# Kernel tuning notes

Measured on AMD Instinct MI355X. Metric: run time of the kernel, lower is better.

The kernel has to match this reference:

```python
import jax, jax.numpy as jnp
import numpy as np
import math

B, S, D, H, L, DFF, V = 4, 1024, 512, 8, 4, 2048, 32000
DK = D // H
SPARSITY = 0.3
K = max(1, int(S * SPARSITY))  # 307
EPS = 1e-5


def _layernorm(x, g, b):
    mu = jnp.mean(x, axis=-1, keepdims=True)
    var = jnp.mean(jnp.square(x - mu), axis=-1, keepdims=True)
    return (x - mu) * jax.lax.rsqrt(var + EPS) * g + b


def _scatter_topk(scores, k):
    # scores: [B,H,S,S]. keep top-k per row, others -inf (torch.topk + scatter_)
    vals, idx = jax.lax.top_k(scores, k)
    lead = int(np.prod(scores.shape[:-1]))
    sk = scores.shape[-1]
    sparse = jnp.full((lead, sk), -jnp.inf, dtype=scores.dtype)
    rows = jnp.arange(lead)[:, None]
    sparse = sparse.at[rows, idx.reshape(lead, k)].set(vals.reshape(lead, k))
    return sparse.reshape(scores.shape)


def _forward(x, tok_emb, pos_emb, Wq, bq, Wk, bk, Wv, bv, Wo, bo,
             g1, be1, g2, be2, W1, b1, Wm, bm, W2, b2, Wout, bout):
    h = tok_emb[x] + pos_emb[jnp.arange(S)][None, :, :]  # [B,S,D]
    scale = 1.0 / math.sqrt(DK)
    for l in range(L):
        y = _layernorm(h, g1[l], be1[l])
        q = (y @ Wq[l] + bq[l]).reshape(B, S, H, DK).transpose(0, 2, 1, 3)
        kk = (y @ Wk[l] + bk[l]).reshape(B, S, H, DK).transpose(0, 2, 1, 3)
        v = (y @ Wv[l] + bv[l]).reshape(B, S, H, DK).transpose(0, 2, 1, 3)
        scores = jnp.einsum('bhqd,bhkd->bhqk', q, kk) * scale
        sparse = _scatter_topk(scores, K)
        attn = jax.nn.softmax(sparse, axis=-1)
        o = jnp.einsum('bhqk,bhkd->bhqd', attn, v)
        o = o.transpose(0, 2, 1, 3).reshape(B, S, D) @ Wo[l] + bo[l]
        h = h + o
        z = _layernorm(h, g2[l], be2[l])
        f = jax.nn.gelu(z @ W1[l] + b1[l], approximate=False)
        f = jax.nn.gelu(f @ Wm[l] + bm[l], approximate=False)
        f = f @ W2[l] + b2[l]
        h = h + f
    return h @ Wout + bout  # logits [B,S,V]


def setup_inputs() -> dict:
    key = jax.random.key(0)
    ks = iter(jax.random.split(key, 32))
    xa = lambda shape, fan: (jax.random.normal(next(ks), shape, jnp.float32)
                             * math.sqrt(2.0 / fan))
    return {
        'x': jax.random.randint(next(ks), (B, S), 0, V, dtype=jnp.int32),
        'tok_emb': xa((V, D), V + D),
        'pos_emb': xa((S, D), S + D),
        'Wq': xa((L, D, D), 2 * D), 'bq': jnp.zeros((L, D), jnp.float32),
        'Wk': xa((L, D, D), 2 * D), 'bk': jnp.zeros((L, D), jnp.float32),
        'Wv': xa((L, D, D), 2 * D), 'bv': jnp.zeros((L, D), jnp.float32),
        'Wo': xa((L, D, D), 2 * D), 'bo': jnp.zeros((L, D), jnp.float32),
        'g1': jnp.ones((L, D), jnp.float32), 'be1': jnp.zeros((L, D), jnp.float32),
        'g2': jnp.ones((L, D), jnp.float32), 'be2': jnp.zeros((L, D), jnp.float32),
        'W1': xa((L, D, DFF), D + DFF), 'b1': jnp.zeros((L, DFF), jnp.float32),
        'Wm': xa((L, DFF, DFF), 2 * DFF), 'bm': jnp.zeros((L, DFF), jnp.float32),
        'W2': xa((L, DFF, D), D + DFF), 'b2': jnp.zeros((L, D), jnp.float32),
        'Wout': xa((D, V), D + V), 'bout': jnp.zeros((V,), jnp.float32),
    }


def reference(x, tok_emb, pos_emb, Wq, bq, Wk, bk, Wv, bv, Wo, bo,
              g1, be1, g2, be2, W1, b1, Wm, bm, W2, b2, Wout, bout):
    return _forward(x, tok_emb, pos_emb, Wq, bq, Wk, bk, Wv, bv, Wo, bo,
                    g1, be1, g2, be2, W1, b1, Wm, bm, W2, b2, Wout, bout)
```

## Files before the change

### kernel.cpp

```cpp
#include <hip/hip_runtime.h>
#include <hip/hip_bf16.h>
#include <math.h>

#define B_ 4
#define S_ 1024
#define D_ 512
#define H_ 8
#define L_ 4
#define DFF_ 2048
#define V_ 32000
#define DK_ 64
#define KTOP 307
#define SRS 1048

using bf16x8 = __attribute__((ext_vector_type(8))) __bf16;
using bf16x4 = __attribute__((ext_vector_type(4))) __bf16;
using bf16x2 = __attribute__((ext_vector_type(2))) __bf16;
using f32x4v = __attribute__((ext_vector_type(4))) float;

__device__ __forceinline__ void gload_lds16(const __bf16* g, __bf16* l) {
  __builtin_amdgcn_global_load_lds(
      (const __attribute__((address_space(1))) void*)g,
      (__attribute__((address_space(3))) void*)l, 16, 0, 0);
}

__device__ __forceinline__ unsigned int f32_to_bf16_bits(float s) {
  unsigned int x = __float_as_uint(s);
  return (x + 0x7FFFu + ((x >> 16) & 1u)) >> 16;
}

__device__ __forceinline__ int red16i(int x) {
  x += __builtin_amdgcn_update_dpp(0, x, 0xB1, 0xF, 0xF, true);
  x += __builtin_amdgcn_update_dpp(0, x, 0x4E, 0xF, 0xF, true);
  x += __builtin_amdgcn_update_dpp(0, x, 0x141, 0xF, 0xF, true);
  x += __builtin_amdgcn_update_dpp(0, x, 0x140, 0xF, 0xF, true);
  return x;
}
__device__ __forceinline__ unsigned int red16umax(unsigned int x) {
  unsigned int t;
  t = (unsigned int)__builtin_amdgcn_update_dpp(0, (int)x, 0xB1, 0xF, 0xF, true);  x = t > x ? t : x;
  t = (unsigned int)__builtin_amdgcn_update_dpp(0, (int)x, 0x4E, 0xF, 0xF, true);  x = t > x ? t : x;
  t = (unsigned int)__builtin_amdgcn_update_dpp(0, (int)x, 0x141, 0xF, 0xF, true); x = t > x ? t : x;
  t = (unsigned int)__builtin_amdgcn_update_dpp(0, (int)x, 0x140, 0xF, 0xF, true); x = t > x ? t : x;
  return x;
}
__device__ __forceinline__ float red16f(float x) {
  x += __int_as_float(__builtin_amdgcn_update_dpp(0, __float_as_int(x), 0xB1, 0xF, 0xF, true));
  x += __int_as_float(__builtin_amdgcn_update_dpp(0, __float_as_int(x), 0x4E, 0xF, 0xF, true));
  x += __int_as_float(__builtin_amdgcn_update_dpp(0, __float_as_int(x), 0x141, 0xF, 0xF, true));
  x += __int_as_float(__builtin_amdgcn_update_dpp(0, __float_as_int(x), 0x140, 0xF, 0xF, true));
  return x;
}
__device__ __forceinline__ float red64f(float x) {
  x = red16f(x);
  x += __shfl_xor(x, 16, 64);
  x += __shfl_xor(x, 32, 64);
  return x;
}

template<int ROWS>
__device__ __forceinline__ void stage_tile4(const __bf16* src, int Kd, __bf16* lds,
                                            int w, int lane) {
  #pragma unroll
  for (int c = 0; c < ROWS / 32; ++c) {
    int rblk = (c * 4 + w) * 8;
    int row = rblk + (lane >> 3);
    int col = (lane & 7) * 8;
    int scol = col ^ ((row & 7) << 3);
    gload_lds16(src + (size_t)row * Kd + scol, lds + rblk * 64);
  }
}
__device__ __forceinline__ void stage_half8(const __bf16* src, int Kd, __bf16* lds,
                                            int w, int lane) {
  #pragma unroll
  for (int c = 0; c < 2; ++c) {
    int rblk = (c * 8 + w) * 8;
    int row = rblk + (lane >> 3);
    int col = (lane & 7) * 8;
    int scol = col ^ ((row & 7) << 3);
    gload_lds16(src + (size_t)row * Kd + scol, lds + rblk * 64);
  }
}
__device__ __forceinline__ bf16x8 lds_frag64(const __bf16* lds, int row, int colbase) {
  int col = colbase ^ ((row & 7) << 3);
  return *reinterpret_cast<const bf16x8*>(lds + row * 64 + col);
}

__global__ void embed_kernel(const int* __restrict__ x, const float* __restrict__ tok,
                             const float* __restrict__ pos, float* __restrict__ h) {
  int row = blockIdx.x;
  int t = threadIdx.x;
  int s = row & (S_ - 1);
  int token = x[row];
  const float4* t4 = reinterpret_cast<const float4*>(tok + (size_t)token * D_);
  const float4* p4 = reinterpret_cast<const float4*>(pos + (size_t)s * D_);
  float4 a = t4[t];
  float4 b = p4[t];
  a.x += b.x; a.y += b.y; a.z += b.z; a.w += b.w;
  reinterpret_cast<float4*>(h + (size_t)row * D_)[t] = a;
}

__global__ void ln_kernel(const float* __restrict__ xin, const float* __restrict__ g,
                          const float* __restrict__ bta, __bf16* __restrict__ y) {
  int row = blockIdx.x;
  int t = threadIdx.x;
  const float2* x2 = reinterpret_cast<const float2*>(xin + (size_t)row * D_);
  float2 v = x2[t];
  float s = v.x + v.y;
  float q = v.x * v.x + v.y * v.y;
  s = red64f(s);
  q = red64f(q);
  __shared__ float red[4];
  __shared__ float red2[4];
  int wid = t >> 6, lane = t & 63;
  if (lane == 0) { red[wid] = s; red2[wid] = q; }
  __syncthreads();
  float mu = (red[0] + red[1] + red[2] + red[3]) * (1.0f / D_);
  float ex2 = (red2[0] + red2[1] + red2[2] + red2[3]) * (1.0f / D_);
  float var = ex2 - mu * mu;
  float rstd = rsqrtf(var + 1e-5f);
  float2 gg = reinterpret_cast<const float2*>(g)[t];
  float2 bb = reinterpret_cast<const float2*>(bta)[t];
  bf16x2 o2;
  o2[0] = (__bf16)((v.x - mu) * rstd * gg.x + bb.x);
  o2[1] = (__bf16)((v.y - mu) * rstd * gg.y + bb.y);
  *reinterpret_cast<bf16x2*>(y + (size_t)row * D_ + t * 2) = o2;
}

__global__ void transpose_bf16_kernel(const float* __restrict__ in, __bf16* __restrict__ out,
                                      int Kd, int N, long in_bstride, long out_bstride) {
  __shared__ float tile[32][33];
  const float* ib = in + (size_t)blockIdx.z * in_bstride;
  __bf16* ob = out + (size_t)blockIdx.z * out_bstride;
  int n0 = blockIdx.x * 32, k0 = blockIdx.y * 32;
  int tx = threadIdx.x & 31, ty = threadIdx.x >> 5;
  #pragma unroll
  for (int i = 0; i < 4; ++i)
    tile[ty + i * 8][tx] = ib[(size_t)(k0 + ty + i * 8) * N + n0 + tx];
  __syncthreads();
  #pragma unroll
  for (int i = 0; i < 4; ++i)
    ob[(size_t)(n0 + ty + i * 8) * Kd + k0 + tx] = (__bf16)tile[tx][ty + i * 8];
}

__global__ void concat_bias_kernel(const float* __restrict__ bq, const float* __restrict__ bk,
                                   const float* __restrict__ bv, float* __restrict__ bqkv) {
  int i = blockIdx.x * 256 + threadIdx.x;
  int l = i / 1536, c = i - l * 1536;
  float v = (c < 512) ? bq[l * 512 + c]
          : (c < 1024) ? bk[l * 512 + c - 512]
                       : bv[l * 512 + c - 1024];
  bqkv[i] = v;
}

#define BM 128
#define BN 128
#define BK 64

template<int OMODE, bool GELU_ACT, bool RES, bool SWZ>
__global__ __launch_bounds__(256)
void gemm_bf16_kernel(const __bf16* __restrict__ A, const __bf16* __restrict__ WT,
                      const float* __restrict__ bias, const float* __restrict__ res,
                      void* __restrict__ outp, void* __restrict__ outp2, void* __restrict__ outp3,
                      int M, int N, int Kd) {
  __shared__ __bf16 As[BM * BK];
  __shared__ __bf16 Ws[BN * BK];
  int tid = threadIdx.x;
  int lane = tid & 63, w = tid >> 6;
  int wr = w >> 1, wc = w & 1;
  int lr = lane & 15, lg = lane >> 4;
  int bx, by;
  if (SWZ) {
    int lid = blockIdx.x;
    int cpx = gridDim.x >> 3;
    int swz = (lid & 7) * cpx + (lid >> 3);
    int gx = M >> 7;
    bx = swz % gx;
    by = swz / gx;
  } else {
    bx = blockIdx.x; by = blockIdx.y;
  }
  int row0 = bx * BM, col0 = by * BN;

  const __bf16* Abase = A + (size_t)row0 * Kd;
  const __bf16* Wbase = WT + (size_t)col0 * Kd;

  f32x4v acc[4][4];
  #pragma unroll
  for (int i = 0; i < 4; ++i)
    #pragma unroll
    for (int j = 0; j < 4; ++j)
      #pragma unroll
      for (int e = 0; e < 4; ++e) acc[i][j][e] = 0.0f;

  for (int k0 = 0; k0 < Kd; k0 += BK) {
    stage_tile4<128>(Abase + k0, Kd, As, w, lane);
    stage_tile4<128>(Wbase + k0, Kd, Ws, w, lane);
    __syncthreads();
    bf16x8 af[4][2], bfr[4][2];
    #pragma unroll
    for (int mr = 0; mr < 4; ++mr)
      #pragma unroll
      for (int kk = 0; kk < 2; ++kk)
        af[mr][kk] = lds_frag64(As, wr * 64 + mr * 16 + lr, kk * 32 + lg * 8);
    #pragma unroll
    for (int nc = 0; nc < 4; ++nc)
      #pragma unroll
      for (int kk = 0; kk < 2; ++kk)
        bfr[nc][kk] = lds_frag64(Ws, wc * 64 + nc * 16 + lr, kk * 32 + lg * 8);
    __builtin_amdgcn_s_setprio(1);
    #pragma unroll
    for (int mr = 0; mr < 4; ++mr)
      #pragma unroll
      for (int nc = 0; nc < 4; ++nc) {
        acc[mr][nc] = __builtin_amdgcn_mfma_f32_16x16x32_bf16(af[mr][0], bfr[nc][0], acc[mr][nc], 0, 0, 0);
        acc[mr][nc] = __builtin_amdgcn_mfma_f32_16x16x32_bf16(af[mr][1], bfr[nc][1], acc[mr][nc], 0, 0, 0);
      }
    __builtin_amdgcn_s_setprio(0);
    __syncthreads();
  }

  #pragma unroll
  for (int mr = 0; mr < 4; ++mr) {
    #pragma unroll
    for (int nc = 0; nc < 4; ++nc) {
      int c = col0 + wc * 64 + nc * 16 + lr;
      int rb = row0 + wr * 64 + mr * 16 + lg * 4;
      float vv[4];
      #pragma unroll
      for (int j = 0; j < 4; ++j) {
        float t = acc[mr][nc][j] + bias[c];
        if (RES) t += res[(size_t)(rb + j) * N + c];
        if (GELU_ACT) t = 0.5f * t * (1.0f + erff(t * 0.70710678118654752f));
        vv[j] = t;
      }
      if (OMODE == 0) {
        float* out = (float*)outp;
        #pragma unroll
        for (int j = 0; j < 4; ++j) out[(size_t)(rb + j) * N + c] = vv[j];
      } else if (OMODE == 1) {
        __bf16* out = (__bf16*)outp;
        #pragma unroll
        for (int j = 0; j < 4; ++j) out[(size_t)(rb + j) * N + c] = (__bf16)vv[j];
      } else if (OMODE == 3) {
        float* out = (float*)outp;
        __bf16* out2 = (__bf16*)outp2;
        #pragma unroll
        for (int j = 0; j < 4; ++j) {
          out[(size_t)(rb + j) * N + c] = vv[j];
          out2[(size_t)(rb + j) * N + c] = (__bf16)vv[j];
        }
      }
    }
  }
}

template<int OMODE, bool RES>
__global__ __launch_bounds__(256)
void gemm64_kernel(const __bf16* __restrict__ A, const __bf16* __restrict__ WT,
                   const float* __restrict__ bias, const float* __restrict__ res,
                   void* __restrict__ outp, void* __restrict__ outp2, void* __restrict__ outp3,
                   int M, int N, int Kd) {
  __shared__ __bf16 As[64 * BK];
  __shared__ __bf16 Ws[BN * BK];
  int tid = threadIdx.x;
  int lane = tid & 63, w = tid >> 6;
  int wr = w >> 1, wc = w & 1;
  int lr = lane & 15, lg = lane >> 4;
  int row0 = blockIdx.x * 64, col0 = blockIdx.y * BN;

  const __bf16* Abase = A + (size_t)row0 * Kd;
  const __bf16* Wbase = WT + (size_t)col0 * Kd;

  f32x4v acc[2][4];
  #pragma unroll
  for (int i = 0; i < 2; ++i)
    #pragma unroll
    for (int j = 0; j < 4; ++j)
      #pragma unroll
      for (int e = 0; e < 4; ++e) acc[i][j][e] = 0.0f;

  for (int k0 = 0; k0 < Kd; k0 += BK) {
    stage_tile4<64>(Abase + k0, Kd, As, w, lane);
    stage_tile4<128>(Wbase + k0, Kd, Ws, w, lane);
    __syncthreads();
    bf16x8 af[2][2], bfr[4][2];
    #pragma unroll
    for (int mr = 0; mr < 2; ++mr)
      #pragma unroll
      for (int kk = 0; kk < 2; ++kk)
        af[mr][kk] = lds_frag64(As, wr * 32 + mr * 16 + lr, kk * 32 + lg * 8);
    #pragma unroll
    for (int nc = 0; nc < 4; ++nc)
      #pragma unroll
      for (int kk = 0; kk < 2; ++kk)
        bfr[nc][kk] = lds_frag64(Ws, wc * 64 + nc * 16 + lr, kk * 32 + lg * 8);
    __builtin_amdgcn_s_setprio(1);
    #pragma unroll
    for (int mr = 0; mr < 2; ++mr)
      #pragma unroll
      for (int nc = 0; nc < 4; ++nc) {
        acc[mr][nc] = __builtin_amdgcn_mfma_f32_16x16x32_bf16(af[mr][0], bfr[nc][0], acc[mr][nc], 0, 0, 0);
        acc[mr][nc] = __builtin_amdgcn_mfma_f32_16x16x32_bf16(af[mr][1], bfr[nc][1], acc[mr][nc], 0, 0, 0);
      }
    __builtin_amdgcn_s_setprio(0);
    __syncthreads();
  }

  #pragma unroll
  for (int mr = 0; mr < 2; ++mr) {
    #pragma unroll
    for (int nc = 0; nc < 4; ++nc) {
      int c = col0 + wc * 64 + nc * 16 + lr;
      int rb = row0 + wr * 32 + mr * 16 + lg * 4;
      float vv[4];
      #pragma unroll
      for (int j = 0; j < 4; ++j) {
        float t = acc[mr][nc][j] + bias[c];
        if (RES) t += res[(size_t)(rb + j) * N + c];
        vv[j] = t;
      }
      if (OMODE == 0) {
        float* out = (float*)outp;
        #pragma unroll
        for (int j = 0; j < 4; ++j) out[(size_t)(rb + j) * N + c] = vv[j];
      } else if (OMODE == 3) {
        float* out = (float*)outp;
        __bf16* out2 = (__bf16*)outp2;
        #pragma unroll
        for (int j = 0; j < 4; ++j) {
          out[(size_t)(rb + j) * N + c] = vv[j];
          out2[(size_t)(rb + j) * N + c] = (__bf16)vv[j];
        }
      } else {
        if (col0 < 512) {
          __bf16* out = (__bf16*)outp;
          #pragma unroll
          for (int j = 0; j < 4; ++j) out[(size_t)(rb + j) * D_ + c] = (__bf16)vv[j];
        } else if (col0 < 1024) {
          __bf16* out = (__bf16*)outp2;
          #pragma unroll
          for (int j = 0; j < 4; ++j) out[(size_t)(rb + j) * D_ + (c - 512)] = (__bf16)vv[j];
        } else {
          __bf16* out = (__bf16*)outp3;
          int b = rb >> 10, s0 = rb & (S_ - 1);
          bf16x4 pk;
          #pragma unroll
          for (int j = 0; j < 4; ++j) pk[j] = (__bf16)vv[j];
          *reinterpret_cast<bf16x4*>(&out[((size_t)b * D_ + (c - 1024)) * S_ + s0]) = pk;
        }
      }
    }
  }
}

__global__ __launch_bounds__(512)
void gemm_head_kernel(const __bf16* __restrict__ A, const __bf16* __restrict__ WT,
                      const float* __restrict__ bias, float* __restrict__ out,
                      int M, int N, int Kd) {
  __shared__ __bf16 lds[2][2][256 * 64];
  const int tid = threadIdx.x;
  const int lane = tid & 63, w = tid >> 6;
  const int wr = w >> 2, wc = w & 3;
  const int lr = lane & 15, lg = lane >> 4;

  int lid = blockIdx.x;
  int cpx = gridDim.x >> 3;
  int swz = (lid & 7) * cpx + (lid >> 3);
  int gx = M >> 8;
  int bx = swz % gx, by = swz / gx;
  int row0 = bx * 256, col0 = by * 256;

  const __bf16* Asrc = A + (size_t)row0 * Kd;
  const __bf16* Bsrc = WT + (size_t)col0 * Kd;

  f32x4v acc[8][4];
  #pragma unroll
  for (int i = 0; i < 8; ++i)
    #pragma unroll
    for (int j = 0; j < 4; ++j)
      #pragma unroll
      for (int e = 0; e < 4; ++e) acc[i][j][e] = 0.0f;

  const int NT = Kd / 64;
  stage_half8(Asrc,                      Kd, &lds[0][0][0],    w, lane);
  stage_half8(Asrc + (size_t)128 * Kd,   Kd, &lds[0][0][8192], w, lane);
  stage_half8(Bsrc,                      Kd, &lds[0][1][0],    w, lane);
  stage_half8(Bsrc + (size_t)128 * Kd,   Kd, &lds[0][1][8192], w, lane);

  for (int t = 0; t < NT; ++t) {
    int cur = t & 1, nxt = cur ^ 1;
    int k1 = (t + 1) * 64;
    const __bf16* Ab = &lds[cur][0][0];
    const __bf16* Bb = &lds[cur][1][0];
    bf16x8 bfr[4][2];
    #pragma unroll
    for (int p = 0; p < 4; ++p) {
      if (t < NT - 1) {
        const __bf16* s;
        __bf16* d;
        if (p == 0)      { s = Asrc + k1;                    d = &lds[nxt][0][0]; }
        else if (p == 1) { s = Asrc + (size_t)128 * Kd + k1; d = &lds[nxt][0][8192]; }
        else if (p == 2) { s = Bsrc + k1;                    d = &lds[nxt][1][0]; }
        else             { s = Bsrc + (size_t)128 * Kd + k1; d = &lds[nxt][1][8192]; }
        stage_half8(s, Kd, d, w, lane);
      }
      if (p == 0) {
        if (t < NT - 1) asm volatile("s_waitcnt vmcnt(2)" ::: "memory");
        else            asm volatile("s_waitcnt vmcnt(0)" ::: "memory");
        __builtin_amdgcn_s_barrier();
        #pragma unroll
        for (int nn = 0; nn < 4; ++nn)
          #pragma unroll
          for (int kk = 0; kk < 2; ++kk)
            bfr[nn][kk] = lds_frag64(Bb, wc * 64 + nn * 16 + lr, kk * 32 + lg * 8);
      }
      bf16x8 af[2][2];
      #pragma unroll
      for (int mm = 0; mm < 2; ++mm)
        #pragma unroll
        for (int kk = 0; kk < 2; ++kk)
          af[mm][kk] = lds_frag64(Ab, wr * 128 + p * 32 + mm * 16 + lr, kk * 32 + lg * 8);
      asm volatile("s_waitcnt lgkmcnt(0)" ::: "memory");
      __builtin_amdgcn_sched_barrier(0);
      __builtin_amdgcn_s_setprio(1);
      #pragma unroll
      for (int mm = 0; mm < 2; ++mm)
        #pragma unroll
        for (int nn = 0; nn < 4; ++nn) {
          acc[p * 2 + mm][nn] = __builtin_amdgcn_mfma_f32_16x16x32_bf16(af[mm][0], bfr[nn][0], acc[p * 2 + mm][nn], 0, 0, 0);
          acc[p * 2 + mm][nn] = __builtin_amdgcn_mfma_f32_16x16x32_bf16(af[mm][1], bfr[nn][1], acc[p * 2 + mm][nn], 0, 0, 0);
        }
      __builtin_amdgcn_s_setprio(0);
    }
    __builtin_amdgcn_s_barrier();
  }

  #pragma unroll
  for (int mg = 0; mg < 8; ++mg) {
    #pragma unroll
    for (int nn = 0; nn < 4; ++nn) {
      int c = col0 + wc * 64 + nn * 16 + lr;
      int rb = row0 + wr * 128 + mg * 16 + lg * 4;
      float b = bias[c];
      #pragma unroll
      for (int j = 0; j < 4; ++j)
        out[(size_t)(rb + j) * N + c] = acc[mg][nn][j] + b;
    }
  }
}

__global__ __launch_bounds__(256)
void attn_kernel(const __bf16* __restrict__ qm, const __bf16* __restrict__ km,
                 const __bf16* __restrict__ vt, __bf16* __restrict__ o) {
  __shared__ unsigned short sc16[16][SRS];
  __shared__ float rs[16];
  const int q0 = blockIdx.x * 16;
  const int hh = blockIdx.y;
  const int bb = blockIdx.z;
  const int tid = threadIdx.x;
  const int lane = tid & 63, w = tid >> 6;
  const int lr = lane & 15, lg = lane >> 4;

  const __bf16* qrow = qm + ((size_t)(bb * S_ + q0 + lr)) * D_ + hh * DK_;
  bf16x8 qf0 = *reinterpret_cast<const bf16x8*>(qrow + lg * 8);
  bf16x8 qf1 = *reinterpret_cast<const bf16x8*>(qrow + 32 + lg * 8);

  const __bf16* kbase = km + ((size_t)bb * S_) * D_ + hh * DK_;
  #pragma unroll 8
  for (int kt = 0; kt < 16; ++kt) {
    int key0 = kt * 64 + w * 16;
    const __bf16* krow = kbase + (size_t)(key0 + lr) * D_;
    bf16x8 kf0 = *reinterpret_cast<const bf16x8*>(krow + lg * 8);
    bf16x8 kf1 = *reinterpret_cast<const bf16x8*>(krow + 32 + lg * 8);
    f32x4v d = {0.0f, 0.0f, 0.0f, 0.0f};
    __builtin_amdgcn_s_setprio(1);
    d = __builtin_amdgcn_mfma_f32_16x16x32_bf16(qf0, kf0, d, 0, 0, 0);
    d = __builtin_amdgcn_mfma_f32_16x16x32_bf16(qf1, kf1, d, 0, 0, 0);
    __builtin_amdgcn_s_setprio(0);
    #pragma unroll
    for (int j = 0; j < 4; ++j) {
      unsigned int u = f32_to_bf16_bits(d[j] * 0.125f);
      u = (u & 0x8000u) ? (~u & 0xFFFFu) : (u | 0x8000u);
      sc16[lg * 4 + j][key0 + lr] = (unsigned short)u;
    }
  }
  __syncthreads();

  {
    int r = tid >> 4, tc = tid & 15;
    const unsigned int* srow = reinterpret_cast<const unsigned int*>(&sc16[r][0]);
    unsigned int wv[32];
    #pragma unroll
    for (int g = 0; g < 8; ++g) {
      uint4 t4 = *reinterpret_cast<const uint4*>(&srow[g * 64 + tc * 4]);
      wv[g * 4 + 0] = t4.x; wv[g * 4 + 1] = t4.y;
      wv[g * 4 + 2] = t4.z; wv[g * 4 + 3] = t4.w;
    }
    unsigned int umax = 0;
    #pragma unroll
    for (int i = 0; i < 32; ++i) {
      unsigned int a = wv[i] & 0xFFFFu, b = wv[i] >> 16;
      unsigned int mx = a > b ? a : b;
      umax = mx > umax ? mx : umax;
    }
    umax = red16umax(umax);
    unsigned int lo = 0;
    for (int bit = 15; bit >= 0; --bit) {
      unsigned int cs = (lo | (1u << bit)) << 16;
      int cnt = 0;
      #pragma unroll
      for (int i = 0; i < 32; ++i) {
        cnt += ((wv[i] << 16) >= cs) ? 1 : 0;
        cnt += (wv[i] >= cs) ? 1 : 0;
      }
      cnt = red16i(cnt);
      if (cnt >= KTOP) lo |= (1u << bit);
    }
    unsigned int um = (umax & 0x8000u) ? (umax ^ 0x8000u) : (~umax & 0xFFFFu);
    float mval = __uint_as_float(um << 16);

    __bf16* P = reinterpret_cast<__bf16*>(&sc16[r][0]);
    float lsum = 0.0f;
    #pragma unroll
    for (int g = 0; g < 8; ++g) {
      bf16x8 pk;
      #pragma unroll
      for (int e = 0; e < 8; ++e) {
        unsigned int wrd = wv[g * 4 + (e >> 1)];
        unsigned int u = (e & 1) ? (wrd >> 16) : (wrd & 0xFFFFu);
        float p = 0.0f;
        if (u >= lo) {
          unsigned int ub = (u & 0x8000u) ? (u ^ 0x8000u) : (~u & 0xFFFFu);
          p = __expf(__uint_as_float(ub << 16) - mval);
        }
        pk[e] = (__bf16)p;
        lsum += (float)pk[e];
      }
      *reinterpret_cast<bf16x8*>(&P[tc * 8 + g * 128]) = pk;
    }
    lsum = red16f(lsum);
    if (tc == 0) rs[r] = 1.0f / lsum;
  }
  __syncthreads();

  {
    const __bf16* P0 = reinterpret_cast<const __bf16*>(&sc16[0][0]);
    const __bf16* vbase = vt + ((size_t)bb * D_ + hh * DK_ + w * 16 + lr) * S_;
    const __bf16* prow = P0 + (size_t)lr * SRS;
    f32x4v oacc = {0.0f, 0.0f, 0.0f, 0.0f};
    __builtin_amdgcn_s_setprio(1);
    #pragma unroll 8
    for (int kt = 0; kt < 32; ++kt) {
      bf16x8 a = *reinterpret_cast<const bf16x8*>(prow + kt * 32 + lg * 8);
      bf16x8 b = *reinterpret_cast<const bf16x8*>(vbase + kt * 32 + lg * 8);
      oacc = __builtin_amdgcn_mfma_f32_16x16x32_bf16(a, b, oacc, 0, 0, 0);
    }
    __builtin_amdgcn_s_setprio(0);
    #pragma unroll
    for (int j = 0; j < 4; ++j) {
      int qr = lg * 4 + j;
      float ov = oacc[j] * rs[qr];
      o[((size_t)(bb * S_ + q0 + qr)) * D_ + hh * DK_ + w * 16 + lr] = (__bf16)ov;
    }
  }
}

extern "C" void kernel_launch(void* const* d_in, const int* in_sizes, int n_in,
                              void* d_out, int out_size, void* d_ws, size_t ws_size,
                              hipStream_t stream) {
  (void)in_sizes; (void)n_in; (void)out_size; (void)ws_size;
  const int*   x    = (const int*)d_in[0];
  const float* tok  = (const float*)d_in[1];
  const float* pos  = (const float*)d_in[2];
  const float* Wq   = (const float*)d_in[3];
  const float* bq   = (const float*)d_in[4];
  const float* Wk   = (const float*)d_in[5];
  const float* bk   = (const float*)d_in[6];
  const float* Wv   = (const float*)d_in[7];
  const float* bv   = (const float*)d_in[8];
  const float* Wo   = (const float*)d_in[9];
  const float* bo   = (const float*)d_in[10];
  const float* g1   = (const float*)d_in[11];
  const float* be1  = (const float*)d_in[12];
  const float* g2   = (const float*)d_in[13];
  const float* be2  = (const float*)d_in[14];
  const float* W1   = (const float*)d_in[15];
  const float* b1   = (const float*)d_in[16];
  const float* Wm   = (const float*)d_in[17];
  const float* bm   = (const float*)d_in[18];
  const float* W2   = (const float*)d_in[19];
  const float* b2   = (const float*)d_in[20];
  const float* Wout = (const float*)d_in[21];
  const float* bout = (const float*)d_in[22];
  float* logits = (float*)d_out;

  const int M = B_ * S_;
  float* ws = (float*)d_ws;
  float* h    = ws;
  float* bqkv = h + (size_t)M * D_;
  __bf16* y16  = (__bf16*)(bqkv + (size_t)L_ * 1536);
  __bf16* f1b  = y16  + (size_t)M * D_;
  __bf16* f2b  = f1b  + (size_t)M * DFF_;
  __bf16* qb16 = f2b  + (size_t)M * DFF_;
  __bf16* kb16 = qb16 + (size_t)M * D_;
  __bf16* vt16 = kb16 + (size_t)M * D_;
  __bf16* ob16 = vt16 + (size_t)M * D_;
  __bf16* h16  = ob16 + (size_t)M * D_;
  __bf16* WqkvT = h16 + (size_t)M * D_;
  __bf16* WoT  = WqkvT + (size_t)L_ * 1536 * D_;
  __bf16* W1T  = WoT  + (size_t)L_ * D_ * D_;
  __bf16* WmT  = W1T  + (size_t)L_ * D_ * DFF_;
  __bf16* W2T  = WmT  + (size_t)L_ * DFF_ * DFF_;
  __bf16* WoutT = W2T + (size_t)L_ * D_ * DFF_;

  const long DD = (long)D_ * D_;
  transpose_bf16_kernel<<<dim3(D_/32,  D_/32,   L_), 256, 0, stream>>>(Wq, WqkvT,            D_, D_, DD, 1536L*D_);
  transpose_bf16_kernel<<<dim3(D_/32,  D_/32,   L_), 256, 0, stream>>>(Wk, WqkvT + 512*512,  D_, D_, DD, 1536L*D_);
  transpose_bf16_kernel<<<dim3(D_/32,  D_/32,   L_), 256, 0, stream>>>(Wv, WqkvT + 1024*512, D_, D_, DD, 1536L*D_);
  transpose_bf16_kernel<<<dim3(D_/32,  D_/32,   L_), 256, 0, stream>>>(Wo, WoT, D_, D_, DD, DD);
  transpose_bf16_kernel<<<dim3(DFF_/32, D_/32,  L_), 256, 0, stream>>>(W1, W1T, D_, DFF_, (long)D_*DFF_, (long)D_*DFF_);
  transpose_bf16_kernel<<<dim3(DFF_/32, DFF_/32,L_), 256, 0, stream>>>(Wm, WmT, DFF_, DFF_, (long)DFF_*DFF_, (long)DFF_*DFF_);
  transpose_bf16_kernel<<<dim3(D_/32,  DFF_/32, L_), 256, 0, stream>>>(W2, W2T, DFF_, D_, (long)D_*DFF_, (long)D_*DFF_);
  transpose_bf16_kernel<<<dim3(V_/32,  D_/32,   1 ), 256, 0, stream>>>(Wout, WoutT, D_, V_, (long)D_*V_, (long)D_*V_);
  concat_bias_kernel<<<(L_*1536)/256, 256, 0, stream>>>(bq, bk, bv, bqkv);

  embed_kernel<<<M, 128, 0, stream>>>(x, tok, pos, h);

  for (int l = 0; l < L_; ++l) {
    ln_kernel<<<M, 256, 0, stream>>>(h, g1 + l * D_, be1 + l * D_, y16);
    gemm64_kernel<4,false><<<dim3(M/64, 1536/BN), 256, 0, stream>>>(
        y16, WqkvT + (size_t)l * 1536 * D_, bqkv + l * 1536, nullptr,
        qb16, kb16, vt16, M, 1536, D_);
    attn_kernel<<<dim3(S_/16, H_, B_), 256, 0, stream>>>(qb16, kb16, vt16, ob16);
    gemm64_kernel<0,true><<<dim3(M/64, D_/BN), 256, 0, stream>>>(
        ob16, WoT + (size_t)l * DD, bo + l * D_, h, h, nullptr, nullptr, M, D_, D_);
    ln_kernel<<<M, 256, 0, stream>>>(h, g2 + l * D_, be2 + l * D_, y16);
    gemm_bf16_kernel<1,true,false,true><<<dim3((M/BM) * (DFF_/BN)), 256, 0, stream>>>(
        y16, W1T + (size_t)l * D_ * DFF_, b1 + l * DFF_, nullptr, f1b, nullptr, nullptr, M, DFF_, D_);
    gemm_bf16_kernel<1,true,false,true><<<dim3((M/BM) * (DFF_/BN)), 256, 0, stream>>>(
        f1b, WmT + (size_t)l * DFF_ * DFF_, bm + l * DFF_, nullptr, f2b, nullptr, nullptr, M, DFF_, DFF_);
    gemm64_kernel<3,true><<<dim3(M/64, D_/BN), 256, 0, stream>>>(
        f2b, W2T + (size_t)l * D_ * DFF_, b2 + l * D_, h, h, h16, nullptr, M, D_, DFF_);
  }
  gemm_head_kernel<<<dim3((M/256) * (V_/256)), 512, 0, stream>>>(
      h16, WoutT, bout, logits, M, V_, D_);
}
```

Measured before the change: 1.251 ms.

## Double attention block threads and use one wave per row in layernorm

The attention kernel goes from 256 to 512 threads per block. QK^T is split across 8 waves, the top-k threshold search and softmax use 32 threads per row with an extra cross-half shuffle, and the PV matmul is split along K into two halves that are reduced through shared memory. This shortens each thread's serial threshold-search and MFMA loops, at the cost of an extra barrier and LDS traffic. Layernorm now handles four rows per block with one wave per row and float4 loads, which removes the shared-memory reduction and barrier.

```diff
diff --git a/kernel.cpp b/kernel.cpp
--- a/kernel.cpp
+++ b/kernel.cpp
@@ -100,31 +100,36 @@
   reinterpret_cast<float4*>(h + (size_t)row * D_)[t] = a;
 }
 
-__global__ void ln_kernel(const float* __restrict__ xin, const float* __restrict__ g,
-                          const float* __restrict__ bta, __bf16* __restrict__ y) {
-  int row = blockIdx.x;
-  int t = threadIdx.x;
-  const float2* x2 = reinterpret_cast<const float2*>(xin + (size_t)row * D_);
-  float2 v = x2[t];
-  float s = v.x + v.y;
-  float q = v.x * v.x + v.y * v.y;
+__global__ __launch_bounds__(256)
+void ln_kernel(const float* __restrict__ xin, const float* __restrict__ g,
+               const float* __restrict__ bta, __bf16* __restrict__ y) {
+  int w = threadIdx.x >> 6, lane = threadIdx.x & 63;
+  int row = blockIdx.x * 4 + w;
+  const float4* x4 = reinterpret_cast<const float4*>(xin + (size_t)row * D_);
+  float4 a = x4[lane * 2];
+  float4 b = x4[lane * 2 + 1];
+  float s = a.x + a.y + a.z + a.w + b.x + b.y + b.z + b.w;
+  float q = a.x * a.x + a.y * a.y + a.z * a.z + a.w * a.w
+          + b.x * b.x + b.y * b.y + b.z * b.z + b.w * b.w;
   s = red64f(s);
   q = red64f(q);
-  __shared__ float red[4];
-  __shared__ float red2[4];
-  int wid = t >> 6, lane = t & 63;
-  if (lane == 0) { red[wid] = s; red2[wid] = q; }
-  __syncthreads();
-  float mu = (red[0] + red[1] + red[2] + red[3]) * (1.0f / D_);
-  float ex2 = (red2[0] + red2[1] + red2[2] + red2[3]) * (1.0f / D_);
-  float var = ex2 - mu * mu;
+  float mu = s * (1.0f / D_);
+  float var = q * (1.0f / D_) - mu * mu;
   float rstd = rsqrtf(var + 1e-5f);
-  float2 gg = reinterpret_cast<const float2*>(g)[t];
-  float2 bb = reinterpret_cast<const float2*>(bta)[t];
-  bf16x2 o2;
-  o2[0] = (__bf16)((v.x - mu) * rstd * gg.x + bb.x);
-  o2[1] = (__bf16)((v.y - mu) * rstd * gg.y + bb.y);
-  *reinterpret_cast<bf16x2*>(y + (size_t)row * D_ + t * 2) = o2;
+  const float4* g4 = reinterpret_cast<const float4*>(g);
+  const float4* b4 = reinterpret_cast<const float4*>(bta);
+  float4 g0 = g4[lane * 2], g1 = g4[lane * 2 + 1];
+  float4 e0 = b4[lane * 2], e1 = b4[lane * 2 + 1];
+  bf16x8 o8;
+  o8[0] = (__bf16)((a.x - mu) * rstd * g0.x + e0.x);
+  o8[1] = (__bf16)((a.y - mu) * rstd * g0.y + e0.y);
+  o8[2] = (__bf16)((a.z - mu) * rstd * g0.z + e0.z);
+  o8[3] = (__bf16)((a.w - mu) * rstd * g0.w + e0.w);
+  o8[4] = (__bf16)((b.x - mu) * rstd * g1.x + e1.x);
+  o8[5] = (__bf16)((b.y - mu) * rstd * g1.y + e1.y);
+  o8[6] = (__bf16)((b.z - mu) * rstd * g1.z + e1.z);
+  o8[7] = (__bf16)((b.w - mu) * rstd * g1.w + e1.w);
+  *reinterpret_cast<bf16x8*>(y + (size_t)row * D_ + lane * 8) = o8;
 }
 
 __global__ void transpose_bf16_kernel(const float* __restrict__ in, __bf16* __restrict__ out,
@@ -450,10 +455,11 @@
   }
 }
 
-__global__ __launch_bounds__(256)
+__global__ __launch_bounds__(512)
 void attn_kernel(const __bf16* __restrict__ qm, const __bf16* __restrict__ km,
                  const __bf16* __restrict__ vt, __bf16* __restrict__ o) {
   __shared__ unsigned short sc16[16][SRS];
+  __shared__ float ored[4][64][4];
   __shared__ float rs[16];
   const int q0 = blockIdx.x * 16;
   const int hh = blockIdx.y;
@@ -467,9 +473,9 @@
   bf16x8 qf1 = *reinterpret_cast<const bf16x8*>(qrow + 32 + lg * 8);
 
   const __bf16* kbase = km + ((size_t)bb * S_) * D_ + hh * DK_;
-  #pragma unroll 8
-  for (int kt = 0; kt < 16; ++kt) {
-    int key0 = kt * 64 + w * 16;
+  #pragma unroll
+  for (int kt = 0; kt < 8; ++kt) {
+    int key0 = kt * 128 + w * 16;
     const __bf16* krow = kbase + (size_t)(key0 + lr) * D_;
     bf16x8 kf0 = *reinterpret_cast<const bf16x8*>(krow + lg * 8);
     bf16x8 kf1 = *reinterpret_cast<const bf16x8*>(krow + 32 + lg * 8);
@@ -488,33 +494,38 @@
   __syncthreads();
 
   {
-    int r = tid >> 4, tc = tid & 15;
+    int r = tid >> 5, tc = tid & 31;
     const unsigned int* srow = reinterpret_cast<const unsigned int*>(&sc16[r][0]);
-    unsigned int wv[32];
-    #pragma unroll
-    for (int g = 0; g < 8; ++g) {
-      uint4 t4 = *reinterpret_cast<const uint4*>(&srow[g * 64 + tc * 4]);
+    unsigned int wv[16];
+    #pragma unroll
+    for (int g = 0; g < 4; ++g) {
+      uint4 t4 = *reinterpret_cast<const uint4*>(&srow[g * 128 + tc * 4]);
       wv[g * 4 + 0] = t4.x; wv[g * 4 + 1] = t4.y;
       wv[g * 4 + 2] = t4.z; wv[g * 4 + 3] = t4.w;
     }
     unsigned int umax = 0;
     #pragma unroll
-    for (int i = 0; i < 32; ++i) {
+    for (int i = 0; i < 16; ++i) {
       unsigned int a = wv[i] & 0xFFFFu, b = wv[i] >> 16;
       unsigned int mx = a > b ? a : b;
       umax = mx > umax ? mx : umax;
     }
     umax = red16umax(umax);
+    {
+      unsigned int other = (unsigned int)__shfl_xor((int)umax, 16, 32);
+      umax = other > umax ? other : umax;
+    }
     unsigned int lo = 0;
     for (int bit = 15; bit >= 0; --bit) {
       unsigned int cs = (lo | (1u << bit)) << 16;
       int cnt = 0;
       #pragma unroll
-      for (int i = 0; i < 32; ++i) {
+      for (int i = 0; i < 16; ++i) {
         cnt += ((wv[i] << 16) >= cs) ? 1 : 0;
         cnt += (wv[i] >= cs) ? 1 : 0;
       }
       cnt = red16i(cnt);
+      cnt += __shfl_xor(cnt, 16, 32);
       if (cnt >= KTOP) lo |= (1u << bit);
     }
     unsigned int um = (umax & 0x8000u) ? (umax ^ 0x8000u) : (~umax & 0xFFFFu);
@@ -523,7 +534,7 @@
     __bf16* P = reinterpret_cast<__bf16*>(&sc16[r][0]);
     float lsum = 0.0f;
     #pragma unroll
-    for (int g = 0; g < 8; ++g) {
+    for (int g = 0; g < 4; ++g) {
       bf16x8 pk;
       #pragma unroll
       for (int e = 0; e < 8; ++e) {
@@ -537,31 +548,46 @@
         pk[e] = (__bf16)p;
         lsum += (float)pk[e];
       }
-      *reinterpret_cast<bf16x8*>(&P[tc * 8 + g * 128]) = pk;
+      *reinterpret_cast<bf16x8*>(&P[tc * 8 + g * 256]) = pk;
     }
     lsum = red16f(lsum);
+    lsum += __shfl_xor(lsum, 16, 32);
     if (tc == 0) rs[r] = 1.0f / lsum;
   }
   __syncthreads();
 
   {
     const __bf16* P0 = reinterpret_cast<const __bf16*>(&sc16[0][0]);
-    const __bf16* vbase = vt + ((size_t)bb * D_ + hh * DK_ + w * 16 + lr) * S_;
+    int wc4 = w & 3;
+    int half = w >> 2;
+    const __bf16* vbase = vt + ((size_t)bb * D_ + hh * DK_ + wc4 * 16 + lr) * S_;
     const __bf16* prow = P0 + (size_t)lr * SRS;
     f32x4v oacc = {0.0f, 0.0f, 0.0f, 0.0f};
+    int kt0 = half * 16;
     __builtin_amdgcn_s_setprio(1);
-    #pragma unroll 8
-    for (int kt = 0; kt < 32; ++kt) {
+    #pragma unroll
+    for (int kk = 0; kk < 16; ++kk) {
+      int kt = kt0 + kk;
       bf16x8 a = *reinterpret_cast<const bf16x8*>(prow + kt * 32 + lg * 8);
       bf16x8 b = *reinterpret_cast<const bf16x8*>(vbase + kt * 32 + lg * 8);
       oacc = __builtin_amdgcn_mfma_f32_16x16x32_bf16(a, b, oacc, 0, 0, 0);
     }
     __builtin_amdgcn_s_setprio(0);
-    #pragma unroll
-    for (int j = 0; j < 4; ++j) {
-      int qr = lg * 4 + j;
-      float ov = oacc[j] * rs[qr];
-      o[((size_t)(bb * S_ + q0 + qr)) * D_ + hh * DK_ + w * 16 + lr] = (__bf16)ov;
+    if (half == 1) {
+      float4 st;
+      st.x = oacc[0]; st.y = oacc[1]; st.z = oacc[2]; st.w = oacc[3];
+      *reinterpret_cast<float4*>(&ored[wc4][lane][0]) = st;
+    }
+    __syncthreads();
+    if (half == 0) {
+      float4 pv = *reinterpret_cast<const float4*>(&ored[wc4][lane][0]);
+      oacc[0] += pv.x; oacc[1] += pv.y; oacc[2] += pv.z; oacc[3] += pv.w;
+      #pragma unroll
+      for (int j = 0; j < 4; ++j) {
+        int qr = lg * 4 + j;
+        float ov = oacc[j] * rs[qr];
+        o[((size_t)(bb * S_ + q0 + qr)) * D_ + hh * DK_ + wc4 * 16 + lr] = (__bf16)ov;
+      }
     }
   }
 }
@@ -628,14 +654,14 @@
   embed_kernel<<<M, 128, 0, stream>>>(x, tok, pos, h);
 
   for (int l = 0; l < L_; ++l) {
-    ln_kernel<<<M, 256, 0, stream>>>(h, g1 + l * D_, be1 + l * D_, y16);
+    ln_kernel<<<M/4, 256, 0, stream>>>(h, g1 + l * D_, be1 + l * D_, y16);
     gemm64_kernel<4,false><<<dim3(M/64, 1536/BN), 256, 0, stream>>>(
         y16, WqkvT + (size_t)l * 1536 * D_, bqkv + l * 1536, nullptr,
         qb16, kb16, vt16, M, 1536, D_);
-    attn_kernel<<<dim3(S_/16, H_, B_), 256, 0, stream>>>(qb16, kb16, vt16, ob16);
+    attn_kernel<<<dim3(S_/16, H_, B_), 512, 0, stream>>>(qb16, kb16, vt16, ob16);
     gemm64_kernel<0,true><<<dim3(M/64, D_/BN), 256, 0, stream>>>(
         ob16, WoT + (size_t)l * DD, bo + l * D_, h, h, nullptr, nullptr, M, D_, D_);
-    ln_kernel<<<M, 256, 0, stream>>>(h, g2 + l * D_, be2 + l * D_, y16);
+    ln_kernel<<<M/4, 256, 0, stream>>>(h, g2 + l * D_, be2 + l * D_, y16);
     gemm_bf16_kernel<1,true,false,true><<<dim3((M/BM) * (DFF_/BN)), 256, 0, stream>>>(
         y16, W1T + (size_t)l * D_ * DFF_, b1 + l * DFF_, nullptr, f1b, nullptr, nullptr, M, DFF_, D_);
     gemm_bf16_kernel<1,true,false,true><<<dim3((M/BM) * (DFF_/BN)), 256, 0, stream>>>(
```

New measurement: 1.211 ms. 1.03x faster.
